# Kernel tuning notes

Hardware: AMD Instinct MI355X
Metric: run time of the kernel (lower is better)

## Reference

```python
import jax, jax.numpy as jnp
import numpy as np

DIM = 1024
NUM_HEADS = 16
HEAD_DIM = DIM // NUM_HEADS
SCALE = HEAD_DIM ** -0.5


def setup_inputs() -> dict:
    key = jax.random.key(0)
    ks = jax.random.split(key, 7)
    s = DIM ** -0.5
    return {
        "x": jax.random.normal(ks[0], (4, 2048, DIM), dtype=jnp.float32),
        "wq": jax.random.normal(ks[1], (DIM, DIM), dtype=jnp.float32) * s,
        "wk": jax.random.normal(ks[2], (DIM, DIM), dtype=jnp.float32) * s,
        "wv": jax.random.normal(ks[3], (DIM, DIM), dtype=jnp.float32) * s,
        "wo": jax.random.normal(ks[4], (DIM, DIM), dtype=jnp.float32) * s,
        "bo": jax.random.normal(ks[5], (DIM,), dtype=jnp.float32) * 0.02,
    }


def reference(x, wq, wk, wv, wo, bo):
    B, N, C = x.shape
    H, D = NUM_HEADS, HEAD_DIM
    # projections (qkv_bias=False); weights stored as [out, in] like nn.Linear
    q = jnp.einsum("bnc,oc->bno", x, wq).reshape(B, N, H, D).transpose(0, 2, 1, 3)
    k = jnp.einsum("bnc,oc->bno", x, wk).reshape(B, N, H, D).transpose(0, 2, 1, 3)
    v = jnp.einsum("bnc,oc->bno", x, wv).reshape(B, N, H, D).transpose(0, 2, 1, 3)
    # full NxN scores, scaled after the matmul as in the original
    scores = jnp.einsum("bhqd,bhkd->bhqk", q, k) * SCALE
    probs = jax.nn.softmax(scores, axis=-1)  # attn_drop is identity (p=0, eval)
    out = jnp.einsum("bhqk,bhkd->bhqd", probs, v)
    out = out.transpose(0, 2, 1, 3).reshape(B, N, C)
    # output projection with bias; proj_drop identity
    return jnp.einsum("bnc,oc->bno", out, wo) + bo
```

## Files before the change

### kernel.cpp

```cpp
#include <hip/hip_runtime.h>
#include <hip/hip_bf16.h>

typedef unsigned short u16;
typedef __attribute__((ext_vector_type(8))) short short8;
typedef __attribute__((ext_vector_type(4))) float f32x4;

#define LOG2E 1.44269504088896340736f

__device__ __forceinline__ u16 f2bf(float f) {
    unsigned u = __float_as_uint(f);
    u += 0x7fffu + ((u >> 16) & 1u);
    return (u16)(u >> 16);
}

__device__ __forceinline__ unsigned pack_bf2(float a, float b) {
    __hip_bfloat162 t = __float22bfloat162_rn(make_float2(a, b));
    return *(unsigned*)&t;
}

__device__ __forceinline__ void async_cp16(const void* g, void* l) {
    __builtin_amdgcn_global_load_lds(
        (const __attribute__((address_space(1))) unsigned*)g,
        (__attribute__((address_space(3))) unsigned*)l, 16, 0, 0);
}

__global__ void cast_all(const float4* __restrict__ x,
                         const float4* __restrict__ wq, const float4* __restrict__ wk,
                         const float4* __restrict__ wv, const float4* __restrict__ wo,
                         uint2* __restrict__ xb, uint2* __restrict__ wqkv,
                         uint2* __restrict__ wob) {
    long long g = (long long)blockIdx.x * blockDim.x + threadIdx.x;
    const long long XG = (8192LL * 1024) / 4;
    const long long WN = (1024LL * 1024) / 4;
    float4 v;
    uint2* dst;
    if (g < XG) {
        v = x[g];
        dst = xb + g;
    } else {
        long long t = g - XG;
        int s = (int)(t / WN);
        long long r = t - (long long)s * WN;
        const float4* src = (s == 0) ? wq : (s == 1) ? wk : (s == 2) ? wv : wo;
        v = src[r];
        dst = (s < 3) ? (wqkv + (long long)s * WN + r) : (wob + r);
    }
    uint2 p;
    p.x = (unsigned)f2bf(v.x) | ((unsigned)f2bf(v.y) << 16);
    p.y = (unsigned)f2bf(v.z) | ((unsigned)f2bf(v.w) << 16);
    *dst = p;
}

template <int MODE>
__global__ __launch_bounds__(256, 2) void gemm_nt(
    const u16* __restrict__ A, const u16* __restrict__ Bw,
    u16* __restrict__ Qo, u16* __restrict__ Ko, u16* __restrict__ Vto,
    float* __restrict__ Fo, const float* __restrict__ bias, int K) {
    __shared__ u16 As[128 * 64];
    __shared__ u16 Bs[128 * 64];

    const int tid = threadIdx.x;
    const int lane = tid & 63, wave = tid >> 6;
    const int wm = wave >> 1, wn = wave & 1;
    const int quad = lane >> 4, l16 = lane & 15;
    const long long m0 = (long long)blockIdx.y * 128;
    const long long n0 = (long long)blockIdx.x * 128;

    f32x4 acc[4][4];
#pragma unroll
    for (int i = 0; i < 4; i++)
#pragma unroll
        for (int j = 0; j < 4; j++) acc[i][j] = (f32x4){0.f, 0.f, 0.f, 0.f};

    for (int kt = 0; kt < K; kt += 64) {
#pragma unroll
        for (int i = 0; i < 4; i++) {
            int ff = i * 256 + tid;
            int row = ff >> 3, c = ff & 7;
            int gc = c ^ (row & 7);
            async_cp16(A + (m0 + row) * K + kt + gc * 8, &As[ff * 8]);
            async_cp16(Bw + (n0 + row) * K + kt + gc * 8, &Bs[ff * 8]);
        }
        __syncthreads();
#pragma unroll
        for (int ks = 0; ks < 2; ks++) {
            short8 af[4], bfr[4];
#pragma unroll
            for (int t = 0; t < 4; t++) {
                int rowA = wm * 64 + t * 16 + l16;
                int ca = (ks * 4 + quad) ^ (rowA & 7);
                af[t] = *(const short8*)(&As[rowA * 64 + ca * 8]);
                int rowB = wn * 64 + t * 16 + l16;
                int cb = (ks * 4 + quad) ^ (rowB & 7);
                bfr[t] = *(const short8*)(&Bs[rowB * 64 + cb * 8]);
            }
#pragma unroll
            for (int i = 0; i < 4; i++)
#pragma unroll
                for (int j = 0; j < 4; j++)
                    acc[i][j] = __builtin_amdgcn_mfma_f32_16x16x32_bf16(
                        af[i], bfr[j], acc[i][j], 0, 0, 0);
        }
        __syncthreads();
    }

#pragma unroll
    for (int i = 0; i < 4; i++) {
        int mg = (int)m0 + wm * 64 + i * 16 + quad * 4;
#pragma unroll
        for (int j = 0; j < 4; j++) {
            int ng = (int)n0 + wn * 64 + j * 16 + l16;
            f32x4 v = acc[i][j];
            if (MODE == 0) {
                int which = ng >> 10;
                int wi = ng & 1023;
                int h = wi >> 6, d = wi & 63;
                int b = mg >> 11;
                int seq = mg & 2047;
                long long bh = (long long)(b * 16 + h);
                if (which == 0) {
                    u16* dst = Qo + (bh * 2048 + seq) * 64 + d;
#pragma unroll
                    for (int r = 0; r < 4; r++) dst[r * 64] = f2bf(v[r] * 0.125f);
                } else if (which == 1) {
                    u16* dst = Ko + (bh * 2048 + seq) * 64 + d;
#pragma unroll
                    for (int r = 0; r < 4; r++) dst[r * 64] = f2bf(v[r]);
                } else {
                    u16* dst = Vto + (bh * 64 + d) * 2048 + seq;
                    uint2 p;
                    p.x = (unsigned)f2bf(v[0]) | ((unsigned)f2bf(v[1]) << 16);
                    p.y = (unsigned)f2bf(v[2]) | ((unsigned)f2bf(v[3]) << 16);
                    *(uint2*)dst = p;
                }
            } else {
                float* dst = Fo + (long long)mg * 1024 + ng;
                float bb = bias[ng];
#pragma unroll
                for (int r = 0; r < 4; r++) dst[r * 1024] = v[r] + bb;
            }
        }
    }
}

__global__ __launch_bounds__(512, 4) void attn(
    const u16* __restrict__ Q, const u16* __restrict__ Kb,
    const u16* __restrict__ Vt, u16* __restrict__ O) {
    __shared__ u16 Ks[2][64 * 64];
    __shared__ u16 Vs[2][64 * 64];
    __shared__ u16 Ps[8][32 * 72];
    __shared__ float Ls[8][32];

    const int tid = threadIdx.x;
    const int lane = tid & 63, wave = tid >> 6;
    const int quad = lane >> 4, l16 = lane & 15;
    const int qt = blockIdx.x, bh = blockIdx.y;

    const u16* Qh = Q + (long long)bh * 2048 * 64;
    const u16* Kh = Kb + (long long)bh * 2048 * 64;
    const u16* Vh = Vt + (long long)bh * 64 * 2048;
    const int q0 = qt * 256 + wave * 32;

    const int srow = tid >> 3, sc = tid & 7;
    const int sgc = sc ^ (srow & 7);
    const u16* Kg = Kh + srow * 64 + sgc * 8;
    const u16* Vg = Vh + (long long)srow * 2048 + sgc * 8;

    short8 qf[2][2];
#pragma unroll
    for (int tm = 0; tm < 2; tm++)
#pragma unroll
        for (int ks = 0; ks < 2; ks++)
            qf[tm][ks] = *(const short8*)(Qh + (q0 + tm * 16 + l16) * 64 + ks * 32 + quad * 8);

    f32x4 o_acc[2][4];
#pragma unroll
    for (int tm = 0; tm < 2; tm++)
#pragma unroll
        for (int tn = 0; tn < 4; tn++) o_acc[tm][tn] = (f32x4){0.f, 0.f, 0.f, 0.f};
    float lsum[2] = {0.f, 0.f};
    const float NEGC = -12.0f * LOG2E;

    u16* Pw = &Ps[wave][0];
    const int prow0 = l16 * 72;
    const int prow1 = (16 + l16) * 72;

    async_cp16(Kg, &Ks[0][tid * 8]);
    async_cp16(Vg, &Vs[0][tid * 8]);

#pragma unroll 1
    for (int kt = 0; kt < 32; kt++) {
        __syncthreads();
        if (kt < 31) {
            const int nk = (kt + 1) & 1;
            async_cp16(Kg + (kt + 1) * 64 * 64, &Ks[nk][tid * 8]);
            async_cp16(Vg + (kt + 1) * 64, &Vs[nk][tid * 8]);
        }
        const u16* Kc = &Ks[kt & 1][0];
        const u16* Vc = &Vs[kt & 1][0];

        f32x4 s[2][4];
#pragma unroll
        for (int tm = 0; tm < 2; tm++)
#pragma unroll
            for (int tn = 0; tn < 4; tn++) s[tm][tn] = (f32x4){0.f, 0.f, 0.f, 0.f};
#pragma unroll
        for (int ks = 0; ks < 2; ks++) {
            short8 kf[4];
#pragma unroll
            for (int tn = 0; tn < 4; tn++) {
                int row = tn * 16 + l16;
                int ca = (ks * 4 + quad) ^ (row & 7);
                kf[tn] = *(const short8*)(&Kc[row * 64 + ca * 8]);
            }
#pragma unroll
            for (int tm = 0; tm < 2; tm++)
#pragma unroll
                for (int tn = 0; tn < 4; tn++)
                    s[tm][tn] = __builtin_amdgcn_mfma_f32_16x16x32_bf16(
                        kf[tn], qf[tm][ks], s[tm][tn], 0, 0, 0);
        }

#pragma unroll
        for (int tm = 0; tm < 2; tm++) {
            const int prow = (tm == 0) ? prow0 : prow1;
            float part = 0.f;
#pragma unroll
            for (int tn = 0; tn < 4; tn++) {
                f32x4 sv = s[tm][tn];
                float p0 = exp2f(fmaf(sv[0], LOG2E, NEGC));
                float p1 = exp2f(fmaf(sv[1], LOG2E, NEGC));
                float p2 = exp2f(fmaf(sv[2], LOG2E, NEGC));
                float p3 = exp2f(fmaf(sv[3], LOG2E, NEGC));
                part += (p0 + p1) + (p2 + p3);
                uint2 pk;
                pk.x = pack_bf2(p0, p1);
                pk.y = pack_bf2(p2, p3);
                *(uint2*)(&Pw[prow + tn * 16 + quad * 4]) = pk;
            }
            lsum[tm] += part;
        }

#pragma unroll
        for (int ks = 0; ks < 2; ks++) {
            short8 vf[4];
#pragma unroll
            for (int tn = 0; tn < 4; tn++) {
                int row = tn * 16 + l16;
                int cv = (ks * 4 + quad) ^ (row & 7);
                vf[tn] = *(const short8*)(&Vc[row * 64 + cv * 8]);
            }
            short8 pf0 = *(const short8*)(&Pw[prow0 + ks * 32 + quad * 8]);
            short8 pf1 = *(const short8*)(&Pw[prow1 + ks * 32 + quad * 8]);
#pragma unroll
            for (int tn = 0; tn < 4; tn++) {
                o_acc[0][tn] = __builtin_amdgcn_mfma_f32_16x16x32_bf16(
                    pf0, vf[tn], o_acc[0][tn], 0, 0, 0);
                o_acc[1][tn] = __builtin_amdgcn_mfma_f32_16x16x32_bf16(
                    pf1, vf[tn], o_acc[1][tn], 0, 0, 0);
            }
        }
    }

#pragma unroll
    for (int tm = 0; tm < 2; tm++) {
        float l = lsum[tm];
        l += __shfl_xor(l, 16);
        l += __shfl_xor(l, 32);
        if (quad == 0) Ls[wave][tm * 16 + l16] = 1.0f / l;
    }
    f32x4 linv[2];
#pragma unroll
    for (int tm = 0; tm < 2; tm++)
        linv[tm] = *(const f32x4*)(&Ls[wave][tm * 16 + quad * 4]);

    const int b = bh >> 4, h = bh & 15;
#pragma unroll
    for (int tm = 0; tm < 2; tm++)
#pragma unroll
        for (int tn = 0; tn < 4; tn++) {
            int seq = q0 + tm * 16 + quad * 4;
            int c = h * 64 + tn * 16 + l16;
            u16* dst = O + ((long long)(b * 2048 + seq)) * 1024 + c;
#pragma unroll
            for (int r = 0; r < 4; r++)
                dst[r * 1024] = f2bf(o_acc[tm][tn][r] * linv[tm][r]);
        }
}

extern "C" void kernel_launch(void* const* d_in, const int* in_sizes, int n_in,
                              void* d_out, int out_size, void* d_ws, size_t ws_size,
                              hipStream_t stream) {
    const float* x = (const float*)d_in[0];
    const float* wq = (const float*)d_in[1];
    const float* wk = (const float*)d_in[2];
    const float* wv = (const float*)d_in[3];
    const float* wo = (const float*)d_in[4];
    const float* bo = (const float*)d_in[5];
    float* out = (float*)d_out;

    char* ws = (char*)d_ws;
    u16* xb   = (u16*)(ws);
    u16* wqkv = (u16*)(ws + (16LL << 20));
    u16* wob  = (u16*)(ws + (22LL << 20));
    u16* Qb   = (u16*)(ws + (24LL << 20));
    u16* Kbuf = (u16*)(ws + (40LL << 20));
    u16* Vt   = (u16*)(ws + (56LL << 20));
    u16* Ob   = (u16*)(ws + (72LL << 20));

    cast_all<<<12288, 256, 0, stream>>>((const float4*)x, (const float4*)wq,
                                        (const float4*)wk, (const float4*)wv,
                                        (const float4*)wo, (uint2*)xb,
                                        (uint2*)wqkv, (uint2*)wob);

    dim3 g1(24, 64);
    gemm_nt<0><<<g1, 256, 0, stream>>>(xb, wqkv, Qb, Kbuf, Vt, nullptr, nullptr, 1024);

    dim3 g2(8, 64);
    attn<<<g2, 512, 0, stream>>>(Qb, Kbuf, Vt, Ob);

    dim3 g3(8, 64);
    gemm_nt<1><<<g3, 256, 0, stream>>>(Ob, wob, nullptr, nullptr, nullptr, out, bo, 1024);
}
```

Measured before the change: 298.9 us.

## Streamline attention softmax: fold log2e into Q, MFMA row sums, truncating bf16 pack

Folds the log2(e) factor into the Q scale at projection time and seeds the score accumulator with the fixed max offset, so each score needs only a raw exp2. Row sums are computed with an MFMA against a ones vector instead of VALU adds plus shuffles and an LDS reduction. Probabilities are packed to bf16 by truncation with a byte permute instead of round-to-nearest. The P buffer gets an XOR swizzle instead of padding, LDS offsets are precomputed, and the loop is unrolled by two so buffer indices are constants. This trades a small loss of precision from truncation and bf16 sums for less VALU work per tile.

Measured after the change: 248.2 us. 1.2x faster.

```diff
diff --git a/kernel.cpp b/kernel.cpp
--- a/kernel.cpp
+++ b/kernel.cpp
@@ -1,5 +1,4 @@
 #include <hip/hip_runtime.h>
-#include <hip/hip_bf16.h>
 
 typedef unsigned short u16;
 typedef __attribute__((ext_vector_type(8))) short short8;
@@ -13,15 +12,14 @@
     return (u16)(u >> 16);
 }
 
-__device__ __forceinline__ unsigned pack_bf2(float a, float b) {
-    __hip_bfloat162 t = __float22bfloat162_rn(make_float2(a, b));
-    return *(unsigned*)&t;
-}
-
 __device__ __forceinline__ void async_cp16(const void* g, void* l) {
     __builtin_amdgcn_global_load_lds(
         (const __attribute__((address_space(1))) unsigned*)g,
         (__attribute__((address_space(3))) unsigned*)l, 16, 0, 0);
+}
+
+__device__ __forceinline__ unsigned pack_trunc(float a, float b) {
+    return __builtin_amdgcn_perm(__float_as_uint(b), __float_as_uint(a), 0x07060302u);
 }
 
 __global__ void cast_all(const float4* __restrict__ x,
@@ -119,9 +117,10 @@
                 int seq = mg & 2047;
                 long long bh = (long long)(b * 16 + h);
                 if (which == 0) {
+                    const float QS = 0.125f * LOG2E;
                     u16* dst = Qo + (bh * 2048 + seq) * 64 + d;
 #pragma unroll
-                    for (int r = 0; r < 4; r++) dst[r * 64] = f2bf(v[r] * 0.125f);
+                    for (int r = 0; r < 4; r++) dst[r * 64] = f2bf(v[r] * QS);
                 } else if (which == 1) {
                     u16* dst = Ko + (bh * 2048 + seq) * 64 + d;
 #pragma unroll
@@ -148,8 +147,7 @@
     const u16* __restrict__ Vt, u16* __restrict__ O) {
     __shared__ u16 Ks[2][64 * 64];
     __shared__ u16 Vs[2][64 * 64];
-    __shared__ u16 Ps[8][32 * 72];
-    __shared__ float Ls[8][32];
+    __shared__ u16 Ps[8][32 * 64];
 
     const int tid = threadIdx.x;
     const int lane = tid & 63, wave = tid >> 6;
@@ -173,106 +171,103 @@
         for (int ks = 0; ks < 2; ks++)
             qf[tm][ks] = *(const short8*)(Qh + (q0 + tm * 16 + l16) * 64 + ks * 32 + quad * 8);
 
-    f32x4 o_acc[2][4];
-#pragma unroll
-    for (int tm = 0; tm < 2; tm++)
+    u16* Pw = &Ps[wave][0];
+    int pwr[2][4], prd[2][2], kvo[2][4];
+#pragma unroll
+    for (int tm = 0; tm < 2; tm++) {
+        const int qrow = tm * 16 + l16;
+#pragma unroll
+        for (int tn = 0; tn < 4; tn++)
+            pwr[tm][tn] = qrow * 64 + (((tn * 2 + (quad >> 1)) ^ (l16 & 7)) * 8) + 4 * (quad & 1);
+#pragma unroll
+        for (int ks = 0; ks < 2; ks++)
+            prd[tm][ks] = qrow * 64 + (((ks * 4 + quad) ^ (l16 & 7)) * 8);
+    }
+#pragma unroll
+    for (int ks = 0; ks < 2; ks++)
+#pragma unroll
+        for (int tn = 0; tn < 4; tn++) {
+            int row = tn * 16 + l16;
+            kvo[ks][tn] = row * 64 + (((ks * 4 + quad) ^ (row & 7)) * 8);
+        }
+
+    f32x4 o_acc[2][4], lacc[2];
+#pragma unroll
+    for (int tm = 0; tm < 2; tm++) {
+        lacc[tm] = (f32x4){0.f, 0.f, 0.f, 0.f};
 #pragma unroll
         for (int tn = 0; tn < 4; tn++) o_acc[tm][tn] = (f32x4){0.f, 0.f, 0.f, 0.f};
-    float lsum[2] = {0.f, 0.f};
+    }
     const float NEGC = -12.0f * LOG2E;
-
-    u16* Pw = &Ps[wave][0];
-    const int prow0 = l16 * 72;
-    const int prow1 = (16 + l16) * 72;
+    const short BF1 = (short)0x3F80;
+    const short8 ones = {BF1, BF1, BF1, BF1, BF1, BF1, BF1, BF1};
 
     async_cp16(Kg, &Ks[0][tid * 8]);
     async_cp16(Vg, &Vs[0][tid * 8]);
 
+#define ATTN_STEP(KT, BUF)                                                              \
+    do {                                                                                \
+        __syncthreads();                                                                \
+        if ((KT) < 31) {                                                                \
+            async_cp16(Kg + ((KT) + 1) * 4096, &Ks[(BUF) ^ 1][tid * 8]);                \
+            async_cp16(Vg + ((KT) + 1) * 64, &Vs[(BUF) ^ 1][tid * 8]);                  \
+        }                                                                               \
+        const u16* Kc = &Ks[BUF][0];                                                    \
+        const u16* Vc = &Vs[BUF][0];                                                    \
+        f32x4 s[2][4];                                                                  \
+        _Pragma("unroll") for (int tm = 0; tm < 2; tm++)                                \
+            _Pragma("unroll") for (int tn = 0; tn < 4; tn++)                            \
+                s[tm][tn] = (f32x4){NEGC, NEGC, NEGC, NEGC};                            \
+        _Pragma("unroll") for (int ks = 0; ks < 2; ks++) {                              \
+            short8 kf[4];                                                               \
+            _Pragma("unroll") for (int tn = 0; tn < 4; tn++)                            \
+                kf[tn] = *(const short8*)(&Kc[kvo[ks][tn]]);                            \
+            _Pragma("unroll") for (int tm = 0; tm < 2; tm++)                            \
+                _Pragma("unroll") for (int tn = 0; tn < 4; tn++)                        \
+                    s[tm][tn] = __builtin_amdgcn_mfma_f32_16x16x32_bf16(                \
+                        kf[tn], qf[tm][ks], s[tm][tn], 0, 0, 0);                        \
+        }                                                                               \
+        _Pragma("unroll") for (int tm = 0; tm < 2; tm++)                                \
+            _Pragma("unroll") for (int tn = 0; tn < 4; tn++) {                          \
+                f32x4 sv = s[tm][tn];                                                   \
+                float p0 = __builtin_amdgcn_exp2f(sv[0]);                               \
+                float p1 = __builtin_amdgcn_exp2f(sv[1]);                               \
+                float p2 = __builtin_amdgcn_exp2f(sv[2]);                               \
+                float p3 = __builtin_amdgcn_exp2f(sv[3]);                               \
+                uint2 pk;                                                               \
+                pk.x = pack_trunc(p0, p1);                                              \
+                pk.y = pack_trunc(p2, p3);                                              \
+                *(uint2*)(&Pw[pwr[tm][tn]]) = pk;                                       \
+            }                                                                           \
+        _Pragma("unroll") for (int ks = 0; ks < 2; ks++) {                              \
+            short8 vf[4];                                                               \
+            _Pragma("unroll") for (int tn = 0; tn < 4; tn++)                            \
+                vf[tn] = *(const short8*)(&Vc[kvo[ks][tn]]);                            \
+            short8 pf0 = *(const short8*)(&Pw[prd[0][ks]]);                             \
+            short8 pf1 = *(const short8*)(&Pw[prd[1][ks]]);                             \
+            lacc[0] = __builtin_amdgcn_mfma_f32_16x16x32_bf16(pf0, ones, lacc[0], 0, 0, 0); \
+            lacc[1] = __builtin_amdgcn_mfma_f32_16x16x32_bf16(pf1, ones, lacc[1], 0, 0, 0); \
+            _Pragma("unroll") for (int tn = 0; tn < 4; tn++) {                          \
+                o_acc[0][tn] = __builtin_amdgcn_mfma_f32_16x16x32_bf16(                 \
+                    pf0, vf[tn], o_acc[0][tn], 0, 0, 0);                                \
+                o_acc[1][tn] = __builtin_amdgcn_mfma_f32_16x16x32_bf16(                 \
+                    pf1, vf[tn], o_acc[1][tn], 0, 0, 0);                                \
+            }                                                                           \
+        }                                                                               \
+    } while (0)
+
 #pragma unroll 1
-    for (int kt = 0; kt < 32; kt++) {
-        __syncthreads();
-        if (kt < 31) {
-            const int nk = (kt + 1) & 1;
-            async_cp16(Kg + (kt + 1) * 64 * 64, &Ks[nk][tid * 8]);
-            async_cp16(Vg + (kt + 1) * 64, &Vs[nk][tid * 8]);
-        }
-        const u16* Kc = &Ks[kt & 1][0];
-        const u16* Vc = &Vs[kt & 1][0];
-
-        f32x4 s[2][4];
-#pragma unroll
-        for (int tm = 0; tm < 2; tm++)
-#pragma unroll
-            for (int tn = 0; tn < 4; tn++) s[tm][tn] = (f32x4){0.f, 0.f, 0.f, 0.f};
-#pragma unroll
-        for (int ks = 0; ks < 2; ks++) {
-            short8 kf[4];
-#pragma unroll
-            for (int tn = 0; tn < 4; tn++) {
-                int row = tn * 16 + l16;
-                int ca = (ks * 4 + quad) ^ (row & 7);
-                kf[tn] = *(const short8*)(&Kc[row * 64 + ca * 8]);
-            }
-#pragma unroll
-            for (int tm = 0; tm < 2; tm++)
-#pragma unroll
-                for (int tn = 0; tn < 4; tn++)
-                    s[tm][tn] = __builtin_amdgcn_mfma_f32_16x16x32_bf16(
-                        kf[tn], qf[tm][ks], s[tm][tn], 0, 0, 0);
-        }
-
-#pragma unroll
-        for (int tm = 0; tm < 2; tm++) {
-            const int prow = (tm == 0) ? prow0 : prow1;
-            float part = 0.f;
-#pragma unroll
-            for (int tn = 0; tn < 4; tn++) {
-                f32x4 sv = s[tm][tn];
-                float p0 = exp2f(fmaf(sv[0], LOG2E, NEGC));
-                float p1 = exp2f(fmaf(sv[1], LOG2E, NEGC));
-                float p2 = exp2f(fmaf(sv[2], LOG2E, NEGC));
-                float p3 = exp2f(fmaf(sv[3], LOG2E, NEGC));
-                part += (p0 + p1) + (p2 + p3);
-                uint2 pk;
-                pk.x = pack_bf2(p0, p1);
-                pk.y = pack_bf2(p2, p3);
-                *(uint2*)(&Pw[prow + tn * 16 + quad * 4]) = pk;
-            }
-            lsum[tm] += part;
-        }
-
-#pragma unroll
-        for (int ks = 0; ks < 2; ks++) {
-            short8 vf[4];
-#pragma unroll
-            for (int tn = 0; tn < 4; tn++) {
-                int row = tn * 16 + l16;
-                int cv = (ks * 4 + quad) ^ (row & 7);
-                vf[tn] = *(const short8*)(&Vc[row * 64 + cv * 8]);
-            }
-            short8 pf0 = *(const short8*)(&Pw[prow0 + ks * 32 + quad * 8]);
-            short8 pf1 = *(const short8*)(&Pw[prow1 + ks * 32 + quad * 8]);
-#pragma unroll
-            for (int tn = 0; tn < 4; tn++) {
-                o_acc[0][tn] = __builtin_amdgcn_mfma_f32_16x16x32_bf16(
-                    pf0, vf[tn], o_acc[0][tn], 0, 0, 0);
-                o_acc[1][tn] = __builtin_amdgcn_mfma_f32_16x16x32_bf16(
-                    pf1, vf[tn], o_acc[1][tn], 0, 0, 0);
-            }
-        }
-    }
-
-#pragma unroll
-    for (int tm = 0; tm < 2; tm++) {
-        float l = lsum[tm];
-        l += __shfl_xor(l, 16);
-        l += __shfl_xor(l, 32);
-        if (quad == 0) Ls[wave][tm * 16 + l16] = 1.0f / l;
-    }
+    for (int kt = 0; kt < 32; kt += 2) {
+        ATTN_STEP(kt, 0);
+        ATTN_STEP(kt + 1, 1);
+    }
+#undef ATTN_STEP
+
     f32x4 linv[2];
 #pragma unroll
     for (int tm = 0; tm < 2; tm++)
-        linv[tm] = *(const f32x4*)(&Ls[wave][tm * 16 + quad * 4]);
+#pragma unroll
+        for (int r = 0; r < 4; r++) linv[tm][r] = 1.0f / lacc[tm][r];
 
     const int b = bh >> 4, h = bh & 15;
 #pragma unroll
```
